# Optimization experiments

Measured on AMD Instinct MI355X. Metric: run time of the kernel, lower is better.

Reference implementation:

```python
import jax, jax.numpy as jnp
import numpy as np

EMBED_DIM = 1024
ATTN_DIM = 128
B, S = 4, 2048


def setup_inputs() -> dict:
    key = jax.random.key(0)
    k1, k2, k3, k4 = jax.random.split(key, 4)
    embedded = jax.random.normal(k1, (B, S, EMBED_DIM), dtype=jnp.float32)
    # torch nn.Linear weights are [out_features, in_features]
    scale = 1.0 / np.sqrt(EMBED_DIM)
    Wk = jax.random.uniform(k2, (ATTN_DIM, EMBED_DIM), dtype=jnp.float32, minval=-scale, maxval=scale)
    Wq = jax.random.uniform(k3, (ATTN_DIM, EMBED_DIM), dtype=jnp.float32, minval=-scale, maxval=scale)
    Wv = jax.random.uniform(k4, (ATTN_DIM, EMBED_DIM), dtype=jnp.float32, minval=-scale, maxval=scale)
    return {"embedded": embedded, "Wk": Wk, "Wq": Wq, "Wv": Wv}


def reference(embedded, Wk, Wq, Wv):
    # projections (no bias): x @ W.T
    k = jnp.einsum('bse,ae->bsa', embedded, Wk)  # [B,S,A]
    q = jnp.einsum('bse,ae->bsa', embedded, Wq)
    v = jnp.einsum('bse,ae->bsa', embedded, Wv)
    ad = k.shape[-1]
    scores = jnp.einsum('bqa,bka->bqk', q, k) / jnp.sqrt(jnp.float32(ad))  # [B,S,S]
    causal = jnp.tril(jnp.ones((scores.shape[1], scores.shape[1]), dtype=bool))
    scores = jnp.where(causal, scores, -jnp.inf)
    probs = jax.nn.softmax(scores, axis=-1)
    out = jnp.einsum('bqk,bka->bqa', probs, v)
    return jnp.round(out, 4)
```

## Files before the change

kernel.cpp:

```cpp
#include <hip/hip_runtime.h>
#include <hip/hip_bf16.h>
#include <math.h>

#define B 4
#define S 2048
#define E 1024
#define A 128
#define CHUNK 256
#define NCHMAX 8

typedef __attribute__((ext_vector_type(8))) short short8;
typedef __attribute__((ext_vector_type(4))) float floatx4;

static __device__ __forceinline__ short f2bf(float f) {
  union { float f; unsigned u; } c;
  c.f = f;
  unsigned r = (c.u + 0x7fffu + ((c.u >> 16) & 1u)) >> 16;
  return (short)r;
}
static __device__ __forceinline__ unsigned f2bf2(float x, float y) {
  __hip_bfloat162 h = __float22bfloat162_rn(float2{x, y});
  union { __hip_bfloat162 h; unsigned u; } c;
  c.h = h;
  return c.u;
}

__global__ __launch_bounds__(256) void wconv(
    const float* __restrict__ Wq,
    const float* __restrict__ Wk,
    const float* __restrict__ Wv,
    short* __restrict__ Wbf) {
  const int which = blockIdx.y;
  const float* Wp = (which == 0) ? Wq : (which == 1) ? Wk : Wv;
  short* o = Wbf + (size_t)which * A * E;
  const int f = blockIdx.x * 256 + threadIdx.x;
  const float4 v = *(const float4*)&Wp[(size_t)f * 4];
  uint2 p; p.x = f2bf2(v.x, v.y); p.y = f2bf2(v.z, v.w);
  *(uint2*)&o[(size_t)f * 4] = p;
}

#define PJ 72
#define CN 130
__global__ __launch_bounds__(256) void proj_gemm(
    const float* __restrict__ X,
    const short* __restrict__ Wbf,
    short* __restrict__ Qbf,
    short* __restrict__ Kbf,
    short* __restrict__ Vt) {
  __shared__ __align__(16) char smem[27648];
  short* As = (short*)smem;
  short* Bs = (short*)(smem + 9216);
  short* Cs = (short*)smem;

  const int m0 = blockIdx.x * 64;
  const int which = blockIdx.y;
  const short* Wpb = Wbf + (size_t)which * A * E;

  const int tid = threadIdx.x;
  const int wave = tid >> 6;
  const int lane = tid & 63;
  const int mh = wave & 1;
  const int nh = wave >> 1;
  const int l16 = lane & 15;
  const int quad = lane >> 4;

  int arow[4], ac4[4], brow[4], bc8[4];
#pragma unroll
  for (int i = 0; i < 4; ++i) {
    const int fa = tid + i * 256;
    arow[i] = fa >> 4; ac4[i] = fa & 15;
    const int fb = tid + i * 256;
    brow[i] = fb >> 3; bc8[i] = fb & 7;
  }

  floatx4 acc[2][4] = {};
  float4 aplf[4];
  short8 bplf[4];

#pragma unroll
  for (int i = 0; i < 4; ++i) {
    aplf[i] = *(const float4*)&X[(size_t)(m0 + arow[i]) * E + ac4[i] * 4];
    bplf[i] = *(const short8*)&Wpb[(size_t)brow[i] * E + bc8[i] * 8];
  }

  for (int k0 = 0; k0 < E; k0 += 64) {
    __syncthreads();
#pragma unroll
    for (int i = 0; i < 4; ++i) {
      uint2 p; p.x = f2bf2(aplf[i].x, aplf[i].y); p.y = f2bf2(aplf[i].z, aplf[i].w);
      *(uint2*)&As[arow[i] * PJ + ac4[i] * 4] = p;
      *(short8*)&Bs[brow[i] * PJ + bc8[i] * 8] = bplf[i];
    }
    __syncthreads();

    if (k0 + 64 < E) {
#pragma unroll
      for (int i = 0; i < 4; ++i) {
        aplf[i] = *(const float4*)&X[(size_t)(m0 + arow[i]) * E + (k0 + 64) + ac4[i] * 4];
        bplf[i] = *(const short8*)&Wpb[(size_t)brow[i] * E + (k0 + 64) + bc8[i] * 8];
      }
    }

    short8 afr[2][2], bfr[4][2];
#pragma unroll
    for (int ms = 0; ms < 2; ++ms)
#pragma unroll
      for (int ks = 0; ks < 2; ++ks)
        afr[ms][ks] = *(const short8*)&As[(mh * 32 + ms * 16 + l16) * PJ + ks * 32 + quad * 8];
#pragma unroll
    for (int nt = 0; nt < 4; ++nt)
#pragma unroll
      for (int ks = 0; ks < 2; ++ks)
        bfr[nt][ks] = *(const short8*)&Bs[(nh * 64 + nt * 16 + l16) * PJ + ks * 32 + quad * 8];

#pragma unroll
    for (int ms = 0; ms < 2; ++ms)
#pragma unroll
      for (int nt = 0; nt < 4; ++nt)
#pragma unroll
        for (int ks = 0; ks < 2; ++ks)
          acc[ms][nt] = __builtin_amdgcn_mfma_f32_16x16x32_bf16(
              afr[ms][ks], bfr[nt][ks], acc[ms][nt], 0, 0, 0);
  }

  const float qscale = 0.08838834764831845f;
  if (which == 2) {
#pragma unroll
    for (int ms = 0; ms < 2; ++ms) {
#pragma unroll
      for (int nt = 0; nt < 4; ++nt) {
        const int n = nh * 64 + nt * 16 + l16;
        const int mbase = m0 + mh * 32 + ms * 16 + quad * 4;
        const int b = mbase >> 11, s = mbase & (S - 1);
        short4 p;
        p.x = f2bf(acc[ms][nt][0]); p.y = f2bf(acc[ms][nt][1]);
        p.z = f2bf(acc[ms][nt][2]); p.w = f2bf(acc[ms][nt][3]);
        *(short4*)&Vt[((size_t)b * A + n) * S + s] = p;
      }
    }
  } else {
    __syncthreads();
    const float sc = (which == 0) ? qscale : 1.0f;
#pragma unroll
    for (int ms = 0; ms < 2; ++ms)
#pragma unroll
      for (int nt = 0; nt < 4; ++nt)
#pragma unroll
        for (int r = 0; r < 4; ++r)
          Cs[(mh * 32 + ms * 16 + quad * 4 + r) * CN + nh * 64 + nt * 16 + l16] =
              f2bf(acc[ms][nt][r] * sc);
    __syncthreads();
    short* Outp = (which == 0) ? Qbf : Kbf;
#pragma unroll
    for (int i = 0; i < 4; ++i) {
      const int f = tid + i * 256;
      const int row = f >> 4, c8 = f & 15;
      *(short8*)&Outp[(size_t)(m0 + row) * A + c8 * 8] =
          *(const short8*)&Cs[row * CN + c8 * 8];
    }
  }
}

#define LK 132
#define LV 68
__global__ __launch_bounds__(256) void attn_part(
    const short* __restrict__ Qbf,
    const short* __restrict__ Kbf,
    const short* __restrict__ Vt,
    float* __restrict__ Opart,
    float* __restrict__ Lpart) {
  __shared__ short Ks[64 * LK];
  __shared__ short Vs[128 * LV];
  __shared__ short Ps[4][16 * LV];

  const int rev = (int)gridDim.x - 1 - (int)blockIdx.x;
  const int qt = rev >> 3;
  const int chunk = rev & 7;
  const int b = qt >> 5;
  const int q0 = (qt & 31) << 6;
  const int nk = q0 + 64;
  const int kstart = chunk * CHUNK;
  if (kstart >= nk) return;
  const int kend = min(kstart + CHUNK, nk);

  const int tid = threadIdx.x;
  const int wave = tid >> 6;
  const int lane = tid & 63;
  const int l16 = lane & 15;
  const int quad = lane >> 4;

  int krow[4], kc8[4], vrow[4], vc8[4];
#pragma unroll
  for (int i = 0; i < 4; ++i) {
    const int f = tid + i * 256;
    krow[i] = f >> 4; kc8[i] = f & 15;
    vrow[i] = f >> 3; vc8[i] = f & 7;
  }

  short8 qfr[4];
  {
    const size_t qrow = (size_t)(b * S + q0 + wave * 16 + l16);
#pragma unroll
    for (int ks = 0; ks < 4; ++ks)
      qfr[ks] = *(const short8*)&Qbf[qrow * A + ks * 32 + quad * 8];
  }

  float l_acc[4] = {0.f, 0.f, 0.f, 0.f};
  floatx4 oacc[8] = {};

  const int myrow = q0 + wave * 16 + quad * 4;
  const short* Kbase = Kbf + (size_t)b * S * A;
  const short* Vbase = Vt + (size_t)b * A * S;

  short8 kplf[4], vplf[4];
#pragma unroll
  for (int i = 0; i < 4; ++i) {
    kplf[i] = *(const short8*)&Kbase[(size_t)(kstart + krow[i]) * A + kc8[i] * 8];
    vplf[i] = *(const short8*)&Vbase[(size_t)vrow[i] * S + kstart + vc8[i] * 8];
  }

  for (int j0 = kstart; j0 < kend; j0 += 64) {
    __syncthreads();
#pragma unroll
    for (int i = 0; i < 4; ++i) {
      *(short8*)&Ks[krow[i] * LK + kc8[i] * 8] = kplf[i];
      *(short8*)&Vs[vrow[i] * LV + vc8[i] * 8] = vplf[i];
    }
    __syncthreads();

    if (j0 + 64 < kend) {
#pragma unroll
      for (int i = 0; i < 4; ++i) {
        kplf[i] = *(const short8*)&Kbase[(size_t)(j0 + 64 + krow[i]) * A + kc8[i] * 8];
        vplf[i] = *(const short8*)&Vbase[(size_t)vrow[i] * S + j0 + 64 + vc8[i] * 8];
      }
    }

    floatx4 sc[4];
#pragma unroll
    for (int nt = 0; nt < 4; ++nt) {
      floatx4 c = {};
#pragma unroll
      for (int ks = 0; ks < 4; ++ks) {
        const short8 bfr = *(const short8*)&Ks[(nt * 16 + l16) * LK + ks * 32 + quad * 8];
        c = __builtin_amdgcn_mfma_f32_16x16x32_bf16(qfr[ks], bfr, c, 0, 0, 0);
      }
      sc[nt] = c;
    }

#pragma unroll
    for (int nt = 0; nt < 4; ++nt) {
      const int key = j0 + nt * 16 + l16;
#pragma unroll
      for (int r = 0; r < 4; ++r) {
        const float p = (key > myrow + r) ? 0.f : __expf(sc[nt][r]);
        sc[nt][r] = p;
        l_acc[r] += p;
      }
    }

#pragma unroll
    for (int nt = 0; nt < 4; ++nt)
#pragma unroll
      for (int r = 0; r < 4; ++r)
        Ps[wave][(quad * 4 + r) * LV + nt * 16 + l16] = f2bf(sc[nt][r]);

    short8 pfr[2];
#pragma unroll
    for (int ks = 0; ks < 2; ++ks)
      pfr[ks] = *(const short8*)&Ps[wave][l16 * LV + ks * 32 + quad * 8];

#pragma unroll
    for (int nt = 0; nt < 8; ++nt) {
#pragma unroll
      for (int ks = 0; ks < 2; ++ks) {
        const short8 vfr = *(const short8*)&Vs[(nt * 16 + l16) * LV + ks * 32 + quad * 8];
        oacc[nt] = __builtin_amdgcn_mfma_f32_16x16x32_bf16(pfr[ks], vfr, oacc[nt], 0, 0, 0);
      }
    }
  }

  const int slot = qt * NCHMAX + chunk;
  float* op = Opart + (size_t)slot * 64 * 128;
  const int lr4 = wave * 16 + quad * 4;
#pragma unroll
  for (int nt = 0; nt < 8; ++nt)
#pragma unroll
    for (int r = 0; r < 4; ++r)
      op[(lr4 + r) * 128 + nt * 16 + l16] = oacc[nt][r];

#pragma unroll
  for (int r = 0; r < 4; ++r) {
    float l = l_acc[r];
    l += __shfl_xor(l, 1);
    l += __shfl_xor(l, 2);
    l += __shfl_xor(l, 4);
    l += __shfl_xor(l, 8);
    if (l16 == 0) Lpart[slot * 64 + lr4 + r] = l;
  }
}

__global__ __launch_bounds__(256) void attn_reduce(
    const float* __restrict__ Opart,
    const float* __restrict__ Lpart,
    float* __restrict__ Out) {
  const int qt = blockIdx.x;
  const int b = qt >> 5;
  const int q0 = (qt & 31) << 6;
  const int nch = (q0 + 64 + CHUNK - 1) / CHUNK;

  const int tid = threadIdx.x;
  const int lr = tid >> 2;
  const int c0 = (tid & 3) * 32;

  float ltot = 0.f;
  for (int c = 0; c < nch; ++c) ltot += Lpart[(qt * NCHMAX + c) * 64 + lr];
  const float inv = 1.f / ltot;

  float4 acc[8] = {};
  for (int c = 0; c < nch; ++c) {
    const float4* op = (const float4*)
        (Opart + ((size_t)(qt * NCHMAX + c) * 64 + lr) * 128 + c0);
#pragma unroll
    for (int i = 0; i < 8; ++i) {
      const float4 v = op[i];
      acc[i].x += v.x; acc[i].y += v.y; acc[i].z += v.z; acc[i].w += v.w;
    }
  }

  float4* o = (float4*)(Out + (size_t)(b * S + q0 + lr) * A + c0);
#pragma unroll
  for (int i = 0; i < 8; ++i) {
    float4 v = acc[i];
    v.x *= inv; v.y *= inv; v.z *= inv; v.w *= inv;
    o[i] = v;
  }
}

extern "C" void kernel_launch(void* const* d_in, const int* in_sizes, int n_in,
                              void* d_out, int out_size, void* d_ws, size_t ws_size,
                              hipStream_t stream) {
  const float* X  = (const float*)d_in[0];
  const float* Wk = (const float*)d_in[1];
  const float* Wq = (const float*)d_in[2];
  const float* Wv = (const float*)d_in[3];
  float* Out = (float*)d_out;

  const size_t qkv_elems = (size_t)B * S * A;
  short* Qbf = (short*)d_ws;
  short* Kbf = Qbf + qkv_elems;
  short* Vt  = Kbf + qkv_elems;
  float* Opart = (float*)(Vt + qkv_elems);
  float* Lpart = Opart + (size_t)1024 * 64 * 128;
  short* Wbf = (short*)(Lpart + (size_t)1024 * 64);

  wconv<<<dim3(A * E / 4 / 256, 3), 256, 0, stream>>>(Wq, Wk, Wv, Wbf);
  dim3 pgrid(B * S / 64, 3);
  proj_gemm<<<pgrid, 256, 0, stream>>>(X, Wbf, Qbf, Kbf, Vt);
  attn_part<<<(B * S / 64) * NCHMAX, 256, 0, stream>>>(Qbf, Kbf, Vt, Opart, Lpart);
  attn_reduce<<<B * S / 64, 256, 0, stream>>>(Opart, Lpart, Out);
}
```

Before: 132.9 us.

## Fuse split-K attention and reduce into one kernel; convert weights inside projection

The split-key attention kernel and its separate reduction kernel are replaced by one fused kernel. Each block walks the whole causal key range in 128-key tiles and owns one 64-column half of the output, so it normalises and writes the final output directly. This removes the fp32 partial-output write and re-read and one launch. The cost is that each output half recomputes QK^T, and the longest blocks run serially over up to 2048 keys, which worsens load balance compared with the chunked split. The separate weight-conversion kernel is also dropped: proj_gemm now loads fp32 weights and converts them to bf16 while staging them into shared memory.

```diff
diff --git a/kernel.cpp b/kernel.cpp
--- a/kernel.cpp
+++ b/kernel.cpp
@@ -6,8 +6,6 @@
 #define S 2048
 #define E 1024
 #define A 128
-#define CHUNK 256
-#define NCHMAX 8
 
 typedef __attribute__((ext_vector_type(8))) short short8;
 typedef __attribute__((ext_vector_type(4))) float floatx4;
@@ -25,25 +23,13 @@
   return c.u;
 }
 
-__global__ __launch_bounds__(256) void wconv(
-    const float* __restrict__ Wq,
-    const float* __restrict__ Wk,
-    const float* __restrict__ Wv,
-    short* __restrict__ Wbf) {
-  const int which = blockIdx.y;
-  const float* Wp = (which == 0) ? Wq : (which == 1) ? Wk : Wv;
-  short* o = Wbf + (size_t)which * A * E;
-  const int f = blockIdx.x * 256 + threadIdx.x;
-  const float4 v = *(const float4*)&Wp[(size_t)f * 4];
-  uint2 p; p.x = f2bf2(v.x, v.y); p.y = f2bf2(v.z, v.w);
-  *(uint2*)&o[(size_t)f * 4] = p;
-}
-
 #define PJ 72
 #define CN 130
 __global__ __launch_bounds__(256) void proj_gemm(
     const float* __restrict__ X,
-    const short* __restrict__ Wbf,
+    const float* __restrict__ Wq,
+    const float* __restrict__ Wk,
+    const float* __restrict__ Wv,
     short* __restrict__ Qbf,
     short* __restrict__ Kbf,
     short* __restrict__ Vt) {
@@ -54,7 +40,7 @@
 
   const int m0 = blockIdx.x * 64;
   const int which = blockIdx.y;
-  const short* Wpb = Wbf + (size_t)which * A * E;
+  const float* Wp = (which == 0) ? Wq : (which == 1) ? Wk : Wv;
 
   const int tid = threadIdx.x;
   const int wave = tid >> 6;
@@ -64,24 +50,28 @@
   const int l16 = lane & 15;
   const int quad = lane >> 4;
 
-  int arow[4], ac4[4], brow[4], bc8[4];
+  int arow[4], ac4[4], brow[8], bc4[8];
 #pragma unroll
   for (int i = 0; i < 4; ++i) {
     const int fa = tid + i * 256;
     arow[i] = fa >> 4; ac4[i] = fa & 15;
+  }
+#pragma unroll
+  for (int i = 0; i < 8; ++i) {
     const int fb = tid + i * 256;
-    brow[i] = fb >> 3; bc8[i] = fb & 7;
+    brow[i] = fb >> 4; bc4[i] = fb & 15;
   }
 
   floatx4 acc[2][4] = {};
   float4 aplf[4];
-  short8 bplf[4];
-
-#pragma unroll
-  for (int i = 0; i < 4; ++i) {
+  float4 wplf[8];
+
+#pragma unroll
+  for (int i = 0; i < 4; ++i)
     aplf[i] = *(const float4*)&X[(size_t)(m0 + arow[i]) * E + ac4[i] * 4];
-    bplf[i] = *(const short8*)&Wpb[(size_t)brow[i] * E + bc8[i] * 8];
-  }
+#pragma unroll
+  for (int i = 0; i < 8; ++i)
+    wplf[i] = *(const float4*)&Wp[(size_t)brow[i] * E + bc4[i] * 4];
 
   for (int k0 = 0; k0 < E; k0 += 64) {
     __syncthreads();
@@ -89,16 +79,21 @@
     for (int i = 0; i < 4; ++i) {
       uint2 p; p.x = f2bf2(aplf[i].x, aplf[i].y); p.y = f2bf2(aplf[i].z, aplf[i].w);
       *(uint2*)&As[arow[i] * PJ + ac4[i] * 4] = p;
-      *(short8*)&Bs[brow[i] * PJ + bc8[i] * 8] = bplf[i];
+    }
+#pragma unroll
+    for (int i = 0; i < 8; ++i) {
+      uint2 p; p.x = f2bf2(wplf[i].x, wplf[i].y); p.y = f2bf2(wplf[i].z, wplf[i].w);
+      *(uint2*)&Bs[brow[i] * PJ + bc4[i] * 4] = p;
     }
     __syncthreads();
 
     if (k0 + 64 < E) {
 #pragma unroll
-      for (int i = 0; i < 4; ++i) {
+      for (int i = 0; i < 4; ++i)
         aplf[i] = *(const float4*)&X[(size_t)(m0 + arow[i]) * E + (k0 + 64) + ac4[i] * 4];
-        bplf[i] = *(const short8*)&Wpb[(size_t)brow[i] * E + (k0 + 64) + bc8[i] * 8];
-      }
+#pragma unroll
+      for (int i = 0; i < 8; ++i)
+        wplf[i] = *(const float4*)&Wp[(size_t)brow[i] * E + (k0 + 64) + bc4[i] * 4];
     }
 
     short8 afr[2][2], bfr[4][2];
@@ -161,27 +156,25 @@
   }
 }
 
-#define LK 132
-#define LV 68
-__global__ __launch_bounds__(256) void attn_part(
+#define LK2 132
+#define LV2 132
+__global__ __launch_bounds__(256) void attn_fused(
     const short* __restrict__ Qbf,
     const short* __restrict__ Kbf,
     const short* __restrict__ Vt,
-    float* __restrict__ Opart,
-    float* __restrict__ Lpart) {
-  __shared__ short Ks[64 * LK];
-  __shared__ short Vs[128 * LV];
-  __shared__ short Ps[4][16 * LV];
-
-  const int rev = (int)gridDim.x - 1 - (int)blockIdx.x;
-  const int qt = rev >> 3;
-  const int chunk = rev & 7;
-  const int b = qt >> 5;
-  const int q0 = (qt & 31) << 6;
+    float* __restrict__ Out) {
+  __shared__ short Ks[128 * LK2];
+  __shared__ short Vs[64 * LV2];
+  __shared__ short Ps[4][16 * LV2];
+
+  const int idx = (int)blockIdx.x;
+  const int r2 = idx >> 1;
+  const int ah = idx & 1;
+  const int iq = 31 - (r2 >> 2);
+  const int b = r2 & 3;
+  const int q0 = iq << 6;
   const int nk = q0 + 64;
-  const int kstart = chunk * CHUNK;
-  if (kstart >= nk) return;
-  const int kend = min(kstart + CHUNK, nk);
+  const int ntiles = (nk + 127) >> 7;
 
   const int tid = threadIdx.x;
   const int wave = tid >> 6;
@@ -189,12 +182,16 @@
   const int l16 = lane & 15;
   const int quad = lane >> 4;
 
-  int krow[4], kc8[4], vrow[4], vc8[4];
+  int krow[8], kc8[8], vrow[4], vc8[4];
+#pragma unroll
+  for (int i = 0; i < 8; ++i) {
+    const int f = tid + i * 256;
+    krow[i] = f >> 4; kc8[i] = f & 15;
+  }
 #pragma unroll
   for (int i = 0; i < 4; ++i) {
     const int f = tid + i * 256;
-    krow[i] = f >> 4; kc8[i] = f & 15;
-    vrow[i] = f >> 3; vc8[i] = f & 7;
+    vrow[i] = f >> 4; vc8[i] = f & 15;
   }
 
   short8 qfr[4];
@@ -206,50 +203,55 @@
   }
 
   float l_acc[4] = {0.f, 0.f, 0.f, 0.f};
-  floatx4 oacc[8] = {};
+  floatx4 oacc[4] = {};
 
   const int myrow = q0 + wave * 16 + quad * 4;
   const short* Kbase = Kbf + (size_t)b * S * A;
-  const short* Vbase = Vt + (size_t)b * A * S;
-
-  short8 kplf[4], vplf[4];
-#pragma unroll
-  for (int i = 0; i < 4; ++i) {
-    kplf[i] = *(const short8*)&Kbase[(size_t)(kstart + krow[i]) * A + kc8[i] * 8];
-    vplf[i] = *(const short8*)&Vbase[(size_t)vrow[i] * S + kstart + vc8[i] * 8];
-  }
-
-  for (int j0 = kstart; j0 < kend; j0 += 64) {
-    __syncthreads();
-#pragma unroll
-    for (int i = 0; i < 4; ++i) {
-      *(short8*)&Ks[krow[i] * LK + kc8[i] * 8] = kplf[i];
-      *(short8*)&Vs[vrow[i] * LV + vc8[i] * 8] = vplf[i];
-    }
-    __syncthreads();
-
-    if (j0 + 64 < kend) {
-#pragma unroll
-      for (int i = 0; i < 4; ++i) {
-        kplf[i] = *(const short8*)&Kbase[(size_t)(j0 + 64 + krow[i]) * A + kc8[i] * 8];
-        vplf[i] = *(const short8*)&Vbase[(size_t)vrow[i] * S + j0 + 64 + vc8[i] * 8];
-      }
-    }
-
-    floatx4 sc[4];
-#pragma unroll
-    for (int nt = 0; nt < 4; ++nt) {
+  const short* Vbase = Vt + ((size_t)b * A + ah * 64) * S;
+
+  short8 kplf[8], vplf[4];
+#pragma unroll
+  for (int i = 0; i < 8; ++i)
+    kplf[i] = *(const short8*)&Kbase[(size_t)krow[i] * A + kc8[i] * 8];
+#pragma unroll
+  for (int i = 0; i < 4; ++i)
+    vplf[i] = *(const short8*)&Vbase[(size_t)vrow[i] * S + vc8[i] * 8];
+
+  for (int t = 0; t < ntiles; ++t) {
+    const int j0 = t * 128;
+    __syncthreads();
+#pragma unroll
+    for (int i = 0; i < 8; ++i)
+      *(short8*)&Ks[krow[i] * LK2 + kc8[i] * 8] = kplf[i];
+#pragma unroll
+    for (int i = 0; i < 4; ++i)
+      *(short8*)&Vs[vrow[i] * LV2 + vc8[i] * 8] = vplf[i];
+    __syncthreads();
+
+    if (t + 1 < ntiles) {
+      const int jn = j0 + 128;
+#pragma unroll
+      for (int i = 0; i < 8; ++i)
+        kplf[i] = *(const short8*)&Kbase[(size_t)(jn + krow[i]) * A + kc8[i] * 8];
+#pragma unroll
+      for (int i = 0; i < 4; ++i)
+        vplf[i] = *(const short8*)&Vbase[(size_t)vrow[i] * S + jn + vc8[i] * 8];
+    }
+
+    floatx4 sc[8];
+#pragma unroll
+    for (int nt = 0; nt < 8; ++nt) {
       floatx4 c = {};
 #pragma unroll
       for (int ks = 0; ks < 4; ++ks) {
-        const short8 bfr = *(const short8*)&Ks[(nt * 16 + l16) * LK + ks * 32 + quad * 8];
+        const short8 bfr = *(const short8*)&Ks[(nt * 16 + l16) * LK2 + ks * 32 + quad * 8];
         c = __builtin_amdgcn_mfma_f32_16x16x32_bf16(qfr[ks], bfr, c, 0, 0, 0);
       }
       sc[nt] = c;
     }
 
 #pragma unroll
-    for (int nt = 0; nt < 4; ++nt) {
+    for (int nt = 0; nt < 8; ++nt) {
       const int key = j0 + nt * 16 + l16;
 #pragma unroll
       for (int r = 0; r < 4; ++r) {
@@ -260,34 +262,25 @@
     }
 
 #pragma unroll
-    for (int nt = 0; nt < 4; ++nt)
+    for (int nt = 0; nt < 8; ++nt)
 #pragma unroll
       for (int r = 0; r < 4; ++r)
-        Ps[wave][(quad * 4 + r) * LV + nt * 16 + l16] = f2bf(sc[nt][r]);
-
-    short8 pfr[2];
-#pragma unroll
-    for (int ks = 0; ks < 2; ++ks)
-      pfr[ks] = *(const short8*)&Ps[wave][l16 * LV + ks * 32 + quad * 8];
-
-#pragma unroll
-    for (int nt = 0; nt < 8; ++nt) {
-#pragma unroll
-      for (int ks = 0; ks < 2; ++ks) {
-        const short8 vfr = *(const short8*)&Vs[(nt * 16 + l16) * LV + ks * 32 + quad * 8];
+        Ps[wave][(quad * 4 + r) * LV2 + nt * 16 + l16] = f2bf(sc[nt][r]);
+
+    short8 pfr[4];
+#pragma unroll
+    for (int ks = 0; ks < 4; ++ks)
+      pfr[ks] = *(const short8*)&Ps[wave][l16 * LV2 + ks * 32 + quad * 8];
+
+#pragma unroll
+    for (int nt = 0; nt < 4; ++nt) {
+#pragma unroll
+      for (int ks = 0; ks < 4; ++ks) {
+        const short8 vfr = *(const short8*)&Vs[(nt * 16 + l16) * LV2 + ks * 32 + quad * 8];
         oacc[nt] = __builtin_amdgcn_mfma_f32_16x16x32_bf16(pfr[ks], vfr, oacc[nt], 0, 0, 0);
       }
     }
   }
-
-  const int slot = qt * NCHMAX + chunk;
-  float* op = Opart + (size_t)slot * 64 * 128;
-  const int lr4 = wave * 16 + quad * 4;
-#pragma unroll
-  for (int nt = 0; nt < 8; ++nt)
-#pragma unroll
-    for (int r = 0; r < 4; ++r)
-      op[(lr4 + r) * 128 + nt * 16 + l16] = oacc[nt][r];
 
 #pragma unroll
   for (int r = 0; r < 4; ++r) {
@@ -296,44 +289,16 @@
     l += __shfl_xor(l, 2);
     l += __shfl_xor(l, 4);
     l += __shfl_xor(l, 8);
-    if (l16 == 0) Lpart[slot * 64 + lr4 + r] = l;
-  }
-}
-
-__global__ __launch_bounds__(256) void attn_reduce(
-    const float* __restrict__ Opart,
-    const float* __restrict__ Lpart,
-    float* __restrict__ Out) {
-  const int qt = blockIdx.x;
-  const int b = qt >> 5;
-  const int q0 = (qt & 31) << 6;
-  const int nch = (q0 + 64 + CHUNK - 1) / CHUNK;
-
-  const int tid = threadIdx.x;
-  const int lr = tid >> 2;
-  const int c0 = (tid & 3) * 32;
-
-  float ltot = 0.f;
-  for (int c = 0; c < nch; ++c) ltot += Lpart[(qt * NCHMAX + c) * 64 + lr];
-  const float inv = 1.f / ltot;
-
-  float4 acc[8] = {};
-  for (int c = 0; c < nch; ++c) {
-    const float4* op = (const float4*)
-        (Opart + ((size_t)(qt * NCHMAX + c) * 64 + lr) * 128 + c0);
-#pragma unroll
-    for (int i = 0; i < 8; ++i) {
-      const float4 v = op[i];
-      acc[i].x += v.x; acc[i].y += v.y; acc[i].z += v.z; acc[i].w += v.w;
-    }
-  }
-
-  float4* o = (float4*)(Out + (size_t)(b * S + q0 + lr) * A + c0);
-#pragma unroll
-  for (int i = 0; i < 8; ++i) {
-    float4 v = acc[i];
-    v.x *= inv; v.y *= inv; v.z *= inv; v.w *= inv;
-    o[i] = v;
+    l_acc[r] = 1.f / l;
+  }
+#pragma unroll
+  for (int nt = 0; nt < 4; ++nt) {
+    const int col = ah * 64 + nt * 16 + l16;
+#pragma unroll
+    for (int r = 0; r < 4; ++r) {
+      const size_t row = (size_t)(b * S + myrow + r);
+      Out[row * A + col] = oacc[nt][r] * l_acc[r];
+    }
   }
 }
 
@@ -350,13 +315,8 @@
   short* Qbf = (short*)d_ws;
   short* Kbf = Qbf + qkv_elems;
   short* Vt  = Kbf + qkv_elems;
-  float* Opart = (float*)(Vt + qkv_elems);
-  float* Lpart = Opart + (size_t)1024 * 64 * 128;
-  short* Wbf = (short*)(Lpart + (size_t)1024 * 64);
-
-  wconv<<<dim3(A * E / 4 / 256, 3), 256, 0, stream>>>(Wq, Wk, Wv, Wbf);
+
   dim3 pgrid(B * S / 64, 3);
-  proj_gemm<<<pgrid, 256, 0, stream>>>(X, Wbf, Qbf, Kbf, Vt);
-  attn_part<<<(B * S / 64) * NCHMAX, 256, 0, stream>>>(Qbf, Kbf, Vt, Opart, Lpart);
-  attn_reduce<<<B * S / 64, 256, 0, stream>>>(Opart, Lpart, Out);
-}
+  proj_gemm<<<pgrid, 256, 0, stream>>>(X, Wq, Wk, Wv, Qbf, Kbf, Vt);
+  attn_fused<<<(B * S / 64) * 2, 256, 0, stream>>>(Qbf, Kbf, Vt, Out);
+}
```

Result: no change. 134.7 us (+1.4%).
